# Performance work log

Measured on AMD Instinct MI355X. Metric: run time of the kernel, lower is better.

## Reference

```python
import jax, jax.numpy as jnp
import numpy as np

N, E, D, R, L = 30000, 200000, 768, 10, 2
EPS = 1e-5

def setup_inputs() -> dict:
    key = jax.random.key(0)
    ks = jax.random.split(key, 10)
    x = jax.random.normal(ks[0], (N, D), dtype=jnp.float32)
    edge_index = jax.random.randint(ks[1], (2, E), 0, N, dtype=jnp.int64)
    edge_type = jax.random.randint(ks[2], (E,), 0, R, dtype=jnp.int64)
    s = 0.02
    W_rel = jax.random.normal(ks[3], (L, R, D, D), dtype=jnp.float32) * s
    W_root = jax.random.normal(ks[4], (L, D, D), dtype=jnp.float32) * s
    bias = jax.random.normal(ks[5], (L, D), dtype=jnp.float32) * s
    ln_g = jnp.ones((L, D), dtype=jnp.float32)
    ln_b = jnp.zeros((L, D), dtype=jnp.float32)
    return {"x": x, "edge_index": edge_index, "edge_type": edge_type,
            "W_rel": W_rel, "W_root": W_root, "bias": bias,
            "ln_g": ln_g, "ln_b": ln_b}

def _layer_norm(h, g, b):
    mu = jnp.mean(h, axis=-1, keepdims=True)
    var = jnp.mean(jnp.square(h - mu), axis=-1, keepdims=True)
    return (h - mu) * jax.lax.rsqrt(var + EPS) * g + b

def _rgcn_conv(h, src, dst, etype, W_rel, W_root, b):
    # per-relation mean aggregation: segment id = dst * R + relation
    seg = dst * R + etype  # [E]
    msgs = h[src]  # [E, D] irregular gather
    sums = jax.ops.segment_sum(msgs, seg, num_segments=N * R)  # [N*R, D]
    cnts = jax.ops.segment_sum(jnp.ones((E,), h.dtype), seg, num_segments=N * R)
    means = sums / jnp.maximum(cnts, 1.0)[:, None]
    means = means.reshape(N, R, D)
    # linearity: mean_r(W_r x_j) == W_r mean_r(x_j)
    agg = jnp.einsum('nrd,rde->ne', means, W_rel)
    return agg + h @ W_root + b

def reference(x, edge_index, edge_type, W_rel, W_root, bias, ln_g, ln_b):
    src, dst = edge_index[0], edge_index[1]
    h = x
    for i in range(L):
        h_prev = h
        h = _rgcn_conv(h, src, dst, edge_type, W_rel[i], W_root[i], bias[i])
        h = _layer_norm(h, ln_g[i], ln_b[i])
        if i > 0:
            h = h + h_prev  # residual (skipped on first layer, per source)
        # dropout is identity in eval mode
        if i < L - 1:
            h = jax.nn.relu(h)
    return h
```

## Files before the change

### kernel.cpp

```cpp
#include <hip/hip_runtime.h>

#define N_NODES 30000
#define N_EDGES 200000
#define DIM 768
#define N_REL 10
#define N_LAYERS 2
#define LN_EPS 1e-5f
#define W_ELEMS (DIM * DIM)
#define BKS 64
#define NT (DIM / BKS)
#define GT_MAX 1573
#define N_ROOT_TILES ((N_NODES + 127) / 128)
#define GT_ALL (GT_MAX + N_ROOT_TILES)

typedef _Float16 f16;
typedef _Float16 f16x4 __attribute__((ext_vector_type(4)));
typedef _Float16 f16x8 __attribute__((ext_vector_type(8)));
typedef float f32x4 __attribute__((ext_vector_type(4)));

#define GLD(gaddr, laddr)                                                              \
    __builtin_amdgcn_global_load_lds((const __attribute__((address_space(1))) void*)(gaddr), \
                                     (__attribute__((address_space(3))) void*)(laddr), 16, 0, 0)

__global__ void count_kernel(const int* __restrict__ ei, const int* __restrict__ et,
                             int* __restrict__ cnt, int* __restrict__ deg,
                             int* __restrict__ posmap) {
    int e = blockIdx.x * blockDim.x + threadIdx.x;
    if (e >= N_EDGES) return;
    int src = ei[e];
    int dst = ei[N_EDGES + e];
    int r = et[e];
    atomicAdd(&cnt[dst * N_REL + r], 1);
    atomicAdd(&deg[dst], 1);
    posmap[r * N_NODES + src] = 1;
}

#define PSCAN_CHUNK 118
__global__ void posscan_kernel(int* __restrict__ posmap, int* __restrict__ mr) {
    __shared__ int part[256];
    const int r = blockIdx.x;
    int* pm = posmap + (size_t)r * N_NODES;
    const int t = threadIdx.x;
    const int c0 = t * PSCAN_CHUNK;
    int s = 0;
    for (int i = 0; i < PSCAN_CHUNK; ++i) {
        const int idx = c0 + i;
        if (idx < N_NODES && pm[idx] == 1) ++s;
    }
    part[t] = s;
    __syncthreads();
    if (t == 0) {
        int a = 0;
        for (int i = 0; i < 256; ++i) { const int v = part[i]; part[i] = a; a += v; }
        mr[r] = a;
    }
    __syncthreads();
    int a = part[t];
    for (int i = 0; i < PSCAN_CHUNK; ++i) {
        const int idx = c0 + i;
        if (idx < N_NODES && pm[idx] == 1) pm[idx] = a++;
    }
}

#define SCAN_CHUNK 118
__global__ void scan_kernel(const int* __restrict__ deg, int* __restrict__ row_start,
                            int* __restrict__ cursor) {
    __shared__ int part[256];
    __shared__ int off[257];
    const int t = threadIdx.x;
    const int c0 = t * SCAN_CHUNK;
    int s = 0;
    for (int i = 0; i < SCAN_CHUNK; ++i) {
        const int idx = c0 + i;
        if (idx < N_NODES) s += deg[idx];
    }
    part[t] = s;
    __syncthreads();
    if (t == 0) {
        int a = 0;
        for (int i = 0; i < 256; ++i) { off[i] = a; a += part[i]; }
        off[256] = a;
        row_start[N_NODES] = a;
    }
    __syncthreads();
    int a = off[t];
    for (int i = 0; i < SCAN_CHUNK; ++i) {
        const int idx = c0 + i;
        if (idx < N_NODES) {
            row_start[idx] = a;
            cursor[idx] = a;
            a += deg[idx];
        }
    }
}

__global__ void zprep_kernel(const int* __restrict__ mr, int* __restrict__ zbase,
                             int* __restrict__ tile_rel) {
    if (blockIdx.x == 0 && threadIdx.x == 0) {
        int zc = 0, tc = 0;
        for (int r = 0; r < N_REL; ++r) {
            zbase[r] = zc;
            const int nt = (mr[r] + 127) >> 7;
            for (int i = 0; i < nt; ++i) tile_rel[tc + i] = r;
            tc += nt;
            zc += nt << 7;
        }
        for (int i = 0; i < N_ROOT_TILES; ++i) tile_rel[tc + i] = N_REL + i;
    }
}

__global__ void fill_kernel(const int* __restrict__ ei, const int* __restrict__ et,
                            const int* __restrict__ posmap, const int* __restrict__ zbase,
                            int* __restrict__ cursor, int* __restrict__ pack,
                            int* __restrict__ srclist) {
    int e = blockIdx.x * blockDim.x + threadIdx.x;
    if (e >= N_EDGES) return;
    int src = ei[e];
    int dst = ei[N_EDGES + e];
    int r = et[e];
    const int zrow = zbase[r] + posmap[r * N_NODES + src];
    int pos = atomicAdd(&cursor[dst], 1);
    pack[pos] = (r << 24) | zrow;
    srclist[zrow] = src;
}

__global__ void convx_kernel(const float* __restrict__ in, f16* __restrict__ out) {
    int idx = blockIdx.x * blockDim.x + threadIdx.x;
    if (idx >= N_NODES * DIM / 4) return;
    const float4 v = *reinterpret_cast<const float4*>(in + (size_t)idx * 4);
    f16x4 o = {(f16)v.x, (f16)v.y, (f16)v.z, (f16)v.w};
    *reinterpret_cast<f16x4*>(out + (size_t)idx * 4) = o;
}

__global__ void convw_kernel(const float* __restrict__ Wrel, const float* __restrict__ Wroot,
                             f16* __restrict__ WT, int layer) {
    __shared__ float tile[32][33];
    const int s = blockIdx.z;
    const float* src = (s < N_REL) ? (Wrel + ((size_t)layer * N_REL + s) * W_ELEMS)
                                   : (Wroot + (size_t)layer * W_ELEMS);
    const int k0 = blockIdx.x * 32;
    const int j0 = blockIdx.y * 32;
    const int tx = threadIdx.x;
    const int ty = threadIdx.y;
#pragma unroll
    for (int i = 0; i < 4; ++i)
        tile[ty + i * 8][tx] = src[(size_t)(k0 + ty + i * 8) * DIM + j0 + tx];
    __syncthreads();
    f16* dst = WT + (size_t)s * W_ELEMS;
#pragma unroll
    for (int i = 0; i < 4; ++i)
        dst[(size_t)(j0 + ty + i * 8) * DIM + k0 + tx] = (f16)tile[tx][ty + i * 8];
}

__global__ void __launch_bounds__(256)
gemm_kernel(const f16* __restrict__ A, const f16* __restrict__ WT,
            const int* __restrict__ srclist, const int* __restrict__ tile_rel,
            f16* __restrict__ Zout, float* __restrict__ aggout) {
    __shared__ alignas(128) f16 As[2][128 * BKS];
    __shared__ alignas(128) f16 Bs[2][128 * BKS];

    const int nwg = gridDim.x;
    const int orig = blockIdx.x;
    const int qq = nwg >> 3, rr = nwg & 7, xc = orig & 7, oo = orig >> 3;
    const int wg = (xc < rr ? xc * (qq + 1) : rr * (qq + 1) + (xc - rr) * qq) + oo;
    const int gt = wg / 6, jt = wg % 6;

    const int v = tile_rel[gt];
    if (v < 0) return;
    const bool comp = (v < N_REL);
    const int rel = comp ? v : N_REL;

    const int t = threadIdx.x;
    const int wv = t >> 6, lane = t & 63;
    const int wr = wv >> 1, wc = wv & 1;
    const f16* B = WT + (size_t)rel * W_ELEMS + (size_t)(jt * 128) * DIM;

    const f16* gA[4];
    const f16* gB[4];
#pragma unroll
    for (int q = 0; q < 4; ++q) {
        const int chunk = q * 256 + t;
        const int row = chunk >> 3;
        const int gk = (chunk & 7) ^ (row & 7);
        int arow;
        if (comp) {
            arow = srclist[gt * 128 + row];
        } else {
            arow = (v - N_REL) * 128 + row;
            if (arow > N_NODES - 1) arow = N_NODES - 1;
        }
        gA[q] = A + (size_t)arow * DIM + gk * 8;
        gB[q] = B + (size_t)row * DIM + gk * 8;
    }

    f32x4 acc[4][4];
#pragma unroll
    for (int i = 0; i < 4; ++i)
#pragma unroll
        for (int j = 0; j < 4; ++j) acc[i][j] = (f32x4){0.f, 0.f, 0.f, 0.f};

    const int lr16 = lane & 15, lk = lane >> 4, l7 = lane & 7;

#pragma unroll
    for (int q = 0; q < 4; ++q) {
        GLD(gA[q], (char*)As[0] + q * 4096 + wv * 1024);
        GLD(gB[q], (char*)Bs[0] + q * 4096 + wv * 1024);
    }
    __syncthreads();

    for (int ks = 0; ks < NT; ++ks) {
        const int cur = ks & 1;
        if (ks < NT - 1) {
#pragma unroll
            for (int q = 0; q < 4; ++q) {
                GLD(gA[q] + (ks + 1) * BKS, (char*)As[cur ^ 1] + q * 4096 + wv * 1024);
                GLD(gB[q] + (ks + 1) * BKS, (char*)Bs[cur ^ 1] + q * 4096 + wv * 1024);
            }
        }
#pragma unroll
        for (int h = 0; h < 2; ++h) {
            f16x8 a[4], b[4];
            const int cp = (((h << 2) | lk) ^ l7) * 8;
#pragma unroll
            for (int i = 0; i < 4; ++i) {
                a[i] = *(const f16x8*)&As[cur][(wr * 64 + i * 16 + lr16) * BKS + cp];
                b[i] = *(const f16x8*)&Bs[cur][(wc * 64 + i * 16 + lr16) * BKS + cp];
            }
#pragma unroll
            for (int mi = 0; mi < 4; ++mi)
#pragma unroll
                for (int ni = 0; ni < 4; ++ni)
                    acc[mi][ni] =
                        __builtin_amdgcn_mfma_f32_16x16x32_f16(a[mi], b[ni], acc[mi][ni], 0, 0, 0);
        }
        __syncthreads();
    }

    const int lrow = lk * 4, lcol = lr16;
    const int c0 = jt * 128 + wc * 64;
    if (comp) {
#pragma unroll
        for (int mi = 0; mi < 4; ++mi)
#pragma unroll
            for (int q = 0; q < 4; ++q) {
                const int z = gt * 128 + wr * 64 + mi * 16 + lrow + q;
                f16* zp = Zout + (size_t)z * DIM + c0 + lcol;
#pragma unroll
                for (int ni = 0; ni < 4; ++ni) zp[ni * 16] = (f16)acc[mi][ni][q];
            }
    } else {
#pragma unroll
        for (int mi = 0; mi < 4; ++mi)
#pragma unroll
            for (int q = 0; q < 4; ++q) {
                const int row = (v - N_REL) * 128 + wr * 64 + mi * 16 + lrow + q;
                if (row >= N_NODES) continue;
                float* op = aggout + (size_t)row * DIM + c0 + lcol;
#pragma unroll
                for (int ni = 0; ni < 4; ++ni) op[ni * 16] = acc[mi][ni][q];
            }
    }
}

__device__ __forceinline__ float block_reduce3(float v, float* sm) {
#pragma unroll
    for (int o = 32; o > 0; o >>= 1) v += __shfl_down(v, o, 64);
    const int wid = threadIdx.x >> 6;
    const int lane = threadIdx.x & 63;
    __syncthreads();
    if (lane == 0) sm[wid] = v;
    __syncthreads();
    return sm[0] + sm[1] + sm[2];
}

__global__ void __launch_bounds__(192)
gather_ln_kernel(const f16* __restrict__ Z, const int* __restrict__ row_start,
                 const int* __restrict__ pack, const int* __restrict__ cnt,
                 const float* __restrict__ agg, const float* __restrict__ bias,
                 const float* __restrict__ g, const float* __restrict__ beta,
                 const f16* __restrict__ resid16, float* __restrict__ outf32,
                 f16* __restrict__ outf16, int do_relu) {
    __shared__ float sm[3];
    const int dst = blockIdx.x;
    const int t = threadIdx.x;
    const int lo = row_start[dst];
    const int hi = row_start[dst + 1];

    const float4 root = *reinterpret_cast<const float4*>(agg + (size_t)dst * DIM + t * 4);
    float a0 = root.x, a1 = root.y, a2 = root.z, a3 = root.w;
    for (int i = lo; i < hi; ++i) {
        const int p = pack[i];
        const int r = p >> 24;
        const int zrow = p & 0xFFFFFF;
        const float inv = 1.0f / (float)cnt[dst * N_REL + r];
        const f16x4 zv = *reinterpret_cast<const f16x4*>(Z + (size_t)zrow * DIM + t * 4);
        a0 += (float)zv[0] * inv;
        a1 += (float)zv[1] * inv;
        a2 += (float)zv[2] * inv;
        a3 += (float)zv[3] * inv;
    }
    const float4 b4 = *reinterpret_cast<const float4*>(bias + t * 4);
    a0 += b4.x; a1 += b4.y; a2 += b4.z; a3 += b4.w;

    const float mu = block_reduce3(a0 + a1 + a2 + a3, sm) * (1.0f / DIM);
    const float c0 = a0 - mu, c1 = a1 - mu, c2 = a2 - mu, c3 = a3 - mu;
    const float var = block_reduce3(c0 * c0 + c1 * c1 + c2 * c2 + c3 * c3, sm) * (1.0f / DIM);
    const float inv = rsqrtf(var + LN_EPS);

    const float4 g4 = *reinterpret_cast<const float4*>(g + t * 4);
    const float4 be4 = *reinterpret_cast<const float4*>(beta + t * 4);
    float o0 = c0 * inv * g4.x + be4.x;
    float o1 = c1 * inv * g4.y + be4.y;
    float o2 = c2 * inv * g4.z + be4.z;
    float o3 = c3 * inv * g4.w + be4.w;
    if (resid16 != nullptr) {
        const f16x4 rv = *reinterpret_cast<const f16x4*>(resid16 + (size_t)dst * DIM + t * 4);
        o0 += (float)rv[0]; o1 += (float)rv[1]; o2 += (float)rv[2]; o3 += (float)rv[3];
    }
    if (do_relu) {
        o0 = fmaxf(o0, 0.f); o1 = fmaxf(o1, 0.f); o2 = fmaxf(o2, 0.f); o3 = fmaxf(o3, 0.f);
    }
    if (outf32 != nullptr) {
        float4 ov = {o0, o1, o2, o3};
        *reinterpret_cast<float4*>(outf32 + (size_t)dst * DIM + t * 4) = ov;
    }
    if (outf16 != nullptr) {
        f16x4 hv = {(f16)o0, (f16)o1, (f16)o2, (f16)o3};
        *reinterpret_cast<f16x4*>(outf16 + (size_t)dst * DIM + t * 4) = hv;
    }
}

extern "C" void kernel_launch(void* const* d_in, const int* in_sizes, int n_in,
                              void* d_out, int out_size, void* d_ws, size_t ws_size,
                              hipStream_t stream) {
    const float* x      = (const float*)d_in[0];
    const int*   ei     = (const int*)d_in[1];
    const int*   et     = (const int*)d_in[2];
    const float* W_rel  = (const float*)d_in[3];
    const float* W_root = (const float*)d_in[4];
    const float* bias   = (const float*)d_in[5];
    const float* ln_g   = (const float*)d_in[6];
    const float* ln_b   = (const float*)d_in[7];
    float* out = (float*)d_out;

    char* w = (char*)d_ws;
    auto alloc = [&](size_t bytes) -> char* {
        char* p = w;
        w += (bytes + 255) & ~(size_t)255;
        return p;
    };
    f16* hf16      = (f16*)alloc((size_t)N_NODES * DIM * 2);
    f16* WT        = (f16*)alloc((size_t)(N_REL + 1) * W_ELEMS * 2);
    int* cnt       = (int*)alloc((size_t)N_NODES * N_REL * 4);
    int* deg       = (int*)alloc((size_t)N_NODES * 4);
    int* row_start = (int*)alloc((size_t)(N_NODES + 1) * 4);
    int* cursor    = (int*)alloc((size_t)N_NODES * 4);
    int* pack      = (int*)alloc((size_t)N_EDGES * 4);
    int* posmap    = (int*)alloc((size_t)N_REL * N_NODES * 4);
    int* mr        = (int*)alloc(64);
    int* zbase     = (int*)alloc(64);
    int* tile_rel  = (int*)alloc((size_t)GT_ALL * 4);
    int* srclist   = (int*)alloc((size_t)GT_MAX * 128 * 4);
    f16* Zg        = (f16*)w;

    hipMemsetAsync(cnt, 0, (size_t)N_NODES * N_REL * 4, stream);
    hipMemsetAsync(deg, 0, (size_t)N_NODES * 4, stream);
    hipMemsetAsync(posmap, 0xFF, (size_t)N_REL * N_NODES * 4, stream);
    hipMemsetAsync(tile_rel, 0xFF, (size_t)GT_ALL * 4, stream);
    hipMemsetAsync(srclist, 0, (size_t)GT_MAX * 128 * 4, stream);
    count_kernel<<<(N_EDGES + 255) / 256, 256, 0, stream>>>(ei, et, cnt, deg, posmap);
    posscan_kernel<<<N_REL, 256, 0, stream>>>(posmap, mr);
    scan_kernel<<<1, 256, 0, stream>>>(deg, row_start, cursor);
    zprep_kernel<<<1, 64, 0, stream>>>(mr, zbase, tile_rel);
    fill_kernel<<<(N_EDGES + 255) / 256, 256, 0, stream>>>(ei, et, posmap, zbase, cursor,
                                                           pack, srclist);
    convx_kernel<<<(N_NODES * DIM / 4 + 255) / 256, 256, 0, stream>>>(x, hf16);

    for (int l = 0; l < N_LAYERS; ++l) {
        convw_kernel<<<dim3(24, 24, N_REL + 1), dim3(32, 8), 0, stream>>>(W_rel, W_root, WT, l);

        gemm_kernel<<<GT_ALL * 6, 256, 0, stream>>>(hf16, WT, srclist, tile_rel, Zg, out);

        gather_ln_kernel<<<N_NODES, 192, 0, stream>>>(
            Zg, row_start, pack, cnt, out,
            bias + (size_t)l * DIM, ln_g + (size_t)l * DIM, ln_b + (size_t)l * DIM,
            (l > 0) ? hf16 : nullptr,
            (l == N_LAYERS - 1) ? out : nullptr,
            (l < N_LAYERS - 1) ? hf16 : nullptr,
            (l < N_LAYERS - 1) ? 1 : 0);
    }
}
```

Baseline: 1.064 ms.

## Enlarge GEMM tiles to 256x256 with 8 waves and MFMA priority hints

The grouped relation/root GEMM moves from 128x128 tiles with 4 waves to 256x256 tiles with 8 waves (512 threads), each wave computing 128x64. Relation row groups are padded to 256 instead of 128, and the tile bookkeeping, srclist sizing and launch grid change to match. This raises arithmetic intensity per LDS and global load and wraps the MFMA bursts in s_setprio. In exchange it uses 128 KB of LDS per block, adds more padding waste per relation, and produces fewer blocks, which can lower occupancy and make the tail less even.

```diff
diff --git a/kernel.cpp b/kernel.cpp
--- a/kernel.cpp
+++ b/kernel.cpp
@@ -9,9 +9,9 @@
 #define W_ELEMS (DIM * DIM)
 #define BKS 64
 #define NT (DIM / BKS)
-#define GT_MAX 1573
-#define N_ROOT_TILES ((N_NODES + 127) / 128)
-#define GT_ALL (GT_MAX + N_ROOT_TILES)
+#define GT2_MAX 792
+#define N_ROOT_TILES ((N_NODES + 255) / 256)
+#define GT2_ALL (GT2_MAX + N_ROOT_TILES)
 
 typedef _Float16 f16;
 typedef _Float16 f16x4 __attribute__((ext_vector_type(4)));
@@ -100,10 +100,10 @@
         int zc = 0, tc = 0;
         for (int r = 0; r < N_REL; ++r) {
             zbase[r] = zc;
-            const int nt = (mr[r] + 127) >> 7;
+            const int nt = (mr[r] + 255) >> 8;
             for (int i = 0; i < nt; ++i) tile_rel[tc + i] = r;
             tc += nt;
-            zc += nt << 7;
+            zc += nt << 8;
         }
         for (int i = 0; i < N_ROOT_TILES; ++i) tile_rel[tc + i] = N_REL + i;
     }
@@ -152,18 +152,18 @@
         dst[(size_t)(j0 + ty + i * 8) * DIM + k0 + tx] = (f16)tile[tx][ty + i * 8];
 }
 
-__global__ void __launch_bounds__(256)
+__global__ void __launch_bounds__(512, 2)
 gemm_kernel(const f16* __restrict__ A, const f16* __restrict__ WT,
             const int* __restrict__ srclist, const int* __restrict__ tile_rel,
             f16* __restrict__ Zout, float* __restrict__ aggout) {
-    __shared__ alignas(128) f16 As[2][128 * BKS];
-    __shared__ alignas(128) f16 Bs[2][128 * BKS];
+    __shared__ alignas(128) f16 As[2][2][128 * BKS];
+    __shared__ alignas(128) f16 Bs[2][2][128 * BKS];
 
     const int nwg = gridDim.x;
     const int orig = blockIdx.x;
-    const int qq = nwg >> 3, rr = nwg & 7, xc = orig & 7, oo = orig >> 3;
-    const int wg = (xc < rr ? xc * (qq + 1) : rr * (qq + 1) + (xc - rr) * qq) + oo;
-    const int gt = wg / 6, jt = wg % 6;
+    const int q8 = nwg >> 3, r8 = nwg & 7, xc = orig & 7, oo = orig >> 3;
+    const int wg = (xc < r8 ? xc * (q8 + 1) : r8 * (q8 + 1) + (xc - r8) * q8) + oo;
+    const int gt = wg / 3, jt = wg % 3;
 
     const int v = tile_rel[gt];
     if (v < 0) return;
@@ -171,91 +171,105 @@
     const int rel = comp ? v : N_REL;
 
     const int t = threadIdx.x;
-    const int wv = t >> 6, lane = t & 63;
-    const int wr = wv >> 1, wc = wv & 1;
-    const f16* B = WT + (size_t)rel * W_ELEMS + (size_t)(jt * 128) * DIM;
-
-    const f16* gA[4];
-    const f16* gB[4];
-#pragma unroll
-    for (int q = 0; q < 4; ++q) {
-        const int chunk = q * 256 + t;
-        const int row = chunk >> 3;
-        const int gk = (chunk & 7) ^ (row & 7);
-        int arow;
-        if (comp) {
-            arow = srclist[gt * 128 + row];
-        } else {
-            arow = (v - N_REL) * 128 + row;
-            if (arow > N_NODES - 1) arow = N_NODES - 1;
+    const int wid = t >> 6, lane = t & 63;
+    const int wr = wid >> 2, wc = wid & 3;
+    const f16* Bp = WT + (size_t)rel * W_ELEMS + (size_t)(jt * 256) * DIM;
+
+    const f16* gA[2][2];
+    const f16* gB[2][2];
+#pragma unroll
+    for (int h = 0; h < 2; ++h)
+#pragma unroll
+        for (int q = 0; q < 2; ++q) {
+            const int c = q * 512 + t;
+            const int r128 = c >> 3;
+            const int gk = (c & 7) ^ (r128 & 7);
+            const int row = h * 128 + r128;
+            int arow;
+            if (comp) {
+                arow = srclist[gt * 256 + row];
+            } else {
+                arow = (v - N_REL) * 256 + row;
+                if (arow > N_NODES - 1) arow = N_NODES - 1;
+            }
+            gA[h][q] = A + (size_t)arow * DIM + gk * 8;
+            gB[h][q] = Bp + (size_t)row * DIM + gk * 8;
         }
-        gA[q] = A + (size_t)arow * DIM + gk * 8;
-        gB[q] = B + (size_t)row * DIM + gk * 8;
-    }
-
-    f32x4 acc[4][4];
-#pragma unroll
-    for (int i = 0; i < 4; ++i)
+
+#define STAGE(buf, ks)                                                                    \
+    do {                                                                                  \
+        _Pragma("unroll") for (int h = 0; h < 2; ++h) {                                   \
+            _Pragma("unroll") for (int q = 0; q < 2; ++q) {                               \
+                GLD(gA[h][q] + (ks) * BKS, (char*)As[buf][h] + q * 8192 + wid * 1024);    \
+                GLD(gB[h][q] + (ks) * BKS, (char*)Bs[buf][h] + q * 8192 + wid * 1024);    \
+            }                                                                             \
+        }                                                                                 \
+    } while (0)
+
+    f32x4 acc[8][4];
+#pragma unroll
+    for (int i = 0; i < 8; ++i)
 #pragma unroll
         for (int j = 0; j < 4; ++j) acc[i][j] = (f32x4){0.f, 0.f, 0.f, 0.f};
 
     const int lr16 = lane & 15, lk = lane >> 4, l7 = lane & 7;
 
-#pragma unroll
-    for (int q = 0; q < 4; ++q) {
-        GLD(gA[q], (char*)As[0] + q * 4096 + wv * 1024);
-        GLD(gB[q], (char*)Bs[0] + q * 4096 + wv * 1024);
-    }
+    STAGE(0, 0);
     __syncthreads();
 
     for (int ks = 0; ks < NT; ++ks) {
         const int cur = ks & 1;
-        if (ks < NT - 1) {
-#pragma unroll
-            for (int q = 0; q < 4; ++q) {
-                GLD(gA[q] + (ks + 1) * BKS, (char*)As[cur ^ 1] + q * 4096 + wv * 1024);
-                GLD(gB[q] + (ks + 1) * BKS, (char*)Bs[cur ^ 1] + q * 4096 + wv * 1024);
+        if (ks < NT - 1) STAGE(cur ^ 1, ks + 1);
+#pragma unroll
+        for (int h = 0; h < 2; ++h) {
+            const int cp = ((((h << 2) | lk) ^ l7)) * 8;
+            f16x8 b[4];
+#pragma unroll
+            for (int ni = 0; ni < 4; ++ni) {
+                const int col = wc * 64 + ni * 16 + lr16;
+                b[ni] = *(const f16x8*)&Bs[cur][col >> 7][(col & 127) * BKS + cp];
+            }
+#pragma unroll
+            for (int mh = 0; mh < 2; ++mh) {
+                f16x8 a[4];
+#pragma unroll
+                for (int m4 = 0; m4 < 4; ++m4) {
+                    const int lrow = mh * 64 + m4 * 16 + lr16;
+                    a[m4] = *(const f16x8*)&As[cur][wr][lrow * BKS + cp];
+                }
+                __builtin_amdgcn_s_setprio(1);
+#pragma unroll
+                for (int m4 = 0; m4 < 4; ++m4)
+#pragma unroll
+                    for (int ni = 0; ni < 4; ++ni)
+                        acc[mh * 4 + m4][ni] = __builtin_amdgcn_mfma_f32_16x16x32_f16(
+                            a[m4], b[ni], acc[mh * 4 + m4][ni], 0, 0, 0);
+                __builtin_amdgcn_s_setprio(0);
             }
         }
-#pragma unroll
-        for (int h = 0; h < 2; ++h) {
-            f16x8 a[4], b[4];
-            const int cp = (((h << 2) | lk) ^ l7) * 8;
-#pragma unroll
-            for (int i = 0; i < 4; ++i) {
-                a[i] = *(const f16x8*)&As[cur][(wr * 64 + i * 16 + lr16) * BKS + cp];
-                b[i] = *(const f16x8*)&Bs[cur][(wc * 64 + i * 16 + lr16) * BKS + cp];
-            }
-#pragma unroll
-            for (int mi = 0; mi < 4; ++mi)
-#pragma unroll
-                for (int ni = 0; ni < 4; ++ni)
-                    acc[mi][ni] =
-                        __builtin_amdgcn_mfma_f32_16x16x32_f16(a[mi], b[ni], acc[mi][ni], 0, 0, 0);
-        }
         __syncthreads();
     }
-
-    const int lrow = lk * 4, lcol = lr16;
-    const int c0 = jt * 128 + wc * 64;
+#undef STAGE
+
+    const int c0 = jt * 256 + wc * 64;
     if (comp) {
 #pragma unroll
-        for (int mi = 0; mi < 4; ++mi)
+        for (int mi = 0; mi < 8; ++mi)
 #pragma unroll
             for (int q = 0; q < 4; ++q) {
-                const int z = gt * 128 + wr * 64 + mi * 16 + lrow + q;
-                f16* zp = Zout + (size_t)z * DIM + c0 + lcol;
+                const int z = gt * 256 + wr * 128 + mi * 16 + lk * 4 + q;
+                f16* zp = Zout + (size_t)z * DIM + c0 + lr16;
 #pragma unroll
                 for (int ni = 0; ni < 4; ++ni) zp[ni * 16] = (f16)acc[mi][ni][q];
             }
     } else {
 #pragma unroll
-        for (int mi = 0; mi < 4; ++mi)
+        for (int mi = 0; mi < 8; ++mi)
 #pragma unroll
             for (int q = 0; q < 4; ++q) {
-                const int row = (v - N_REL) * 128 + wr * 64 + mi * 16 + lrow + q;
+                const int row = (v - N_REL) * 256 + wr * 128 + mi * 16 + lk * 4 + q;
                 if (row >= N_NODES) continue;
-                float* op = aggout + (size_t)row * DIM + c0 + lcol;
+                float* op = aggout + (size_t)row * DIM + c0 + lr16;
 #pragma unroll
                 for (int ni = 0; ni < 4; ++ni) op[ni * 16] = acc[mi][ni][q];
             }
@@ -359,15 +373,15 @@
     int* posmap    = (int*)alloc((size_t)N_REL * N_NODES * 4);
     int* mr        = (int*)alloc(64);
     int* zbase     = (int*)alloc(64);
-    int* tile_rel  = (int*)alloc((size_t)GT_ALL * 4);
-    int* srclist   = (int*)alloc((size_t)GT_MAX * 128 * 4);
+    int* tile_rel  = (int*)alloc((size_t)GT2_ALL * 4);
+    int* srclist   = (int*)alloc((size_t)GT2_MAX * 256 * 4);
     f16* Zg        = (f16*)w;
 
     hipMemsetAsync(cnt, 0, (size_t)N_NODES * N_REL * 4, stream);
     hipMemsetAsync(deg, 0, (size_t)N_NODES * 4, stream);
     hipMemsetAsync(posmap, 0xFF, (size_t)N_REL * N_NODES * 4, stream);
-    hipMemsetAsync(tile_rel, 0xFF, (size_t)GT_ALL * 4, stream);
-    hipMemsetAsync(srclist, 0, (size_t)GT_MAX * 128 * 4, stream);
+    hipMemsetAsync(tile_rel, 0xFF, (size_t)GT2_ALL * 4, stream);
+    hipMemsetAsync(srclist, 0, (size_t)GT2_MAX * 256 * 4, stream);
     count_kernel<<<(N_EDGES + 255) / 256, 256, 0, stream>>>(ei, et, cnt, deg, posmap);
     posscan_kernel<<<N_REL, 256, 0, stream>>>(posmap, mr);
     scan_kernel<<<1, 256, 0, stream>>>(deg, row_start, cursor);
@@ -379,7 +393,7 @@
     for (int l = 0; l < N_LAYERS; ++l) {
         convw_kernel<<<dim3(24, 24, N_REL + 1), dim3(32, 8), 0, stream>>>(W_rel, W_root, WT, l);
 
-        gemm_kernel<<<GT_ALL * 6, 256, 0, stream>>>(hf16, WT, srclist, tile_rel, Zg, out);
+        gemm_kernel<<<GT2_ALL * 3, 512, 0, stream>>>(hf16, WT, srclist, tile_rel, Zg, out);
 
         gather_ln_kernel<<<N_NODES, 192, 0, stream>>>(
             Zg, row_start, pack, cnt, out,
```

Measured after the change: 1.086 ms. +2.1%, slower.
